# Optimization experiments

Hardware: AMD Instinct MI355X
Metric: run time of the kernel (lower is better)

The kernel has to match this reference:

```python
import jax, jax.numpy as jnp
import numpy as np

NUM_HEADS = 8
OUT_FEATS = 128
D_HEAD = OUT_FEATS // NUM_HEADS
N_NODES = 50000
N_EDGES = 600000
IN_FEATS = 128


def setup_inputs() -> dict:
    key = jax.random.key(0)
    ks = jax.random.split(key, 10)
    h = jax.random.normal(ks[0], (N_NODES, IN_FEATS), dtype=jnp.float32)
    src = jax.random.randint(ks[1], (N_EDGES,), 0, N_NODES)
    dst = jax.random.randint(ks[2], (N_EDGES,), 0, N_NODES)
    s = 1.0 / np.sqrt(IN_FEATS)
    W_Q = jax.random.normal(ks[3], (IN_FEATS, OUT_FEATS), dtype=jnp.float32) * s
    W_K = jax.random.normal(ks[4], (IN_FEATS, OUT_FEATS), dtype=jnp.float32) * s
    W_V = jax.random.normal(ks[5], (IN_FEATS, OUT_FEATS), dtype=jnp.float32) * s
    b_Q = jnp.zeros((OUT_FEATS,), dtype=jnp.float32)
    b_K = jnp.zeros((OUT_FEATS,), dtype=jnp.float32)
    b_V = jnp.zeros((OUT_FEATS,), dtype=jnp.float32)
    return {"h": h, "W_Q": W_Q, "b_Q": b_Q, "W_K": W_K, "b_K": b_K,
            "W_V": W_V, "b_V": b_V, "src": src, "dst": dst}


def _graph_conv(h, W, b, src, dst, norm_src, norm_dst):
    # DGL GraphConv, norm='both': D_dst^{-1/2} * A * D_src^{-1/2} * (h W) + b
    x = (h * norm_src[:, None]) @ W                              # [N, F]
    agg = jax.ops.segment_sum(x[src], dst, num_segments=h.shape[0])
    return agg * norm_dst[:, None] + b


def reference(h, W_Q, b_Q, W_K, b_K, W_V, b_V, src, dst):
    N = h.shape[0]
    ones = jnp.ones(src.shape[0], dtype=h.dtype)
    deg_out = jax.ops.segment_sum(ones, src, num_segments=N)   # out-degree (src side)
    deg_in = jax.ops.segment_sum(ones, dst, num_segments=N)    # in-degree (dst side)
    norm_src = jax.lax.rsqrt(jnp.clip(deg_out, 1.0))
    norm_dst = jax.lax.rsqrt(jnp.clip(deg_in, 1.0))

    Q = jax.nn.relu(_graph_conv(h, W_Q, b_Q, src, dst, norm_src, norm_dst))
    K = jax.nn.relu(_graph_conv(h, W_K, b_K, src, dst, norm_src, norm_dst))
    V = jax.nn.relu(_graph_conv(h, W_V, b_V, src, dst, norm_src, norm_dst))

    Qh = Q.reshape(N, NUM_HEADS, D_HEAD)
    Kh = K.reshape(N, NUM_HEADS, D_HEAD)
    Vh = V.reshape(N, NUM_HEADS, D_HEAD)

    # edge-wise scores: K at src dotted with Q at dst, per head
    score = jnp.sum(Kh[src] * Qh[dst], axis=-1, keepdims=True)   # [E, H, 1]
    score = jnp.exp(jnp.clip(score / np.sqrt(D_HEAD), -10.0, 10.0))

    wV = jax.ops.segment_sum(Vh[src] * score, dst, num_segments=N)  # [N, H, Dh]
    z = jax.ops.segment_sum(score, dst, num_segments=N)             # [N, H, 1]
    return wV / (z + 1e-6)
```

## Files before the change

### kernel.cpp

```cpp
#include <hip/hip_runtime.h>

#define INF  128
#define OUTF 128
#define NH   8
#define DHD  16
#define CAP  48

typedef __attribute__((ext_vector_type(8))) short bf16x8;
typedef __attribute__((ext_vector_type(4))) float f32x4;

__device__ __forceinline__ float bf16_to_f32(unsigned short u) {
    union { unsigned int i; float f; } v;
    v.i = ((unsigned int)u) << 16;
    return v.f;
}
__device__ __forceinline__ unsigned short f32_to_bf16(float f) {
    union { float f; unsigned int i; } v;
    v.f = f;
    unsigned int x = v.i;
    return (unsigned short)((x + 0x7fffu + ((x >> 16) & 1u)) >> 16);
}

__global__ void k_front(const int* __restrict__ src, const int* __restrict__ dst,
                        int* __restrict__ deg_out, int* __restrict__ cursor,
                        int* __restrict__ edge_src, int E, int SB, int HB,
                        const float* __restrict__ h, unsigned short* __restrict__ h_b, int N,
                        const float* __restrict__ Wq, const float* __restrict__ Wk,
                        const float* __restrict__ Wv, unsigned short* __restrict__ frag) {
    if (blockIdx.x < (unsigned)SB) {
        int t = blockIdx.x * 256 + threadIdx.x;
        int e0 = t * 4;
        if (e0 + 4 <= E) {
            int4 s4 = *reinterpret_cast<const int4*>(src + e0);
            int4 d4 = *reinterpret_cast<const int4*>(dst + e0);
            atomicAdd(&deg_out[s4.x], 1);
            atomicAdd(&deg_out[s4.y], 1);
            atomicAdd(&deg_out[s4.z], 1);
            atomicAdd(&deg_out[s4.w], 1);
            int p0 = atomicAdd(&cursor[d4.x], 1);
            int p1 = atomicAdd(&cursor[d4.y], 1);
            int p2 = atomicAdd(&cursor[d4.z], 1);
            int p3 = atomicAdd(&cursor[d4.w], 1);
            if (p0 < CAP) edge_src[d4.x * CAP + p0] = s4.x;
            if (p1 < CAP) edge_src[d4.y * CAP + p1] = s4.y;
            if (p2 < CAP) edge_src[d4.z * CAP + p2] = s4.z;
            if (p3 < CAP) edge_src[d4.w * CAP + p3] = s4.w;
        } else {
            for (int e = e0; e < E; ++e) {
                int s = src[e];
                int d = dst[e];
                atomicAdd(&deg_out[s], 1);
                int p = atomicAdd(&cursor[d], 1);
                if (p < CAP) edge_src[d * CAP + p] = s;
            }
        }
    } else if (blockIdx.x < (unsigned)(SB + HB)) {
        int t = (blockIdx.x - SB) * 256 + threadIdx.x;
        if (t < N * (INF / 8)) {
            const float4* p = reinterpret_cast<const float4*>(h + (size_t)t * 8);
            float4 v0 = p[0], v1 = p[1];
            uint4 o;
            o.x = (unsigned int)f32_to_bf16(v0.x) | ((unsigned int)f32_to_bf16(v0.y) << 16);
            o.y = (unsigned int)f32_to_bf16(v0.z) | ((unsigned int)f32_to_bf16(v0.w) << 16);
            o.z = (unsigned int)f32_to_bf16(v1.x) | ((unsigned int)f32_to_bf16(v1.y) << 16);
            o.w = (unsigned int)f32_to_bf16(v1.z) | ((unsigned int)f32_to_bf16(v1.w) << 16);
            *reinterpret_cast<uint4*>(h_b + (size_t)t * 8) = o;
        }
    } else {
        int t = (blockIdx.x - SB - HB) * 256 + threadIdx.x;
        if (t >= 3 * 8 * 4 * 2 * 64) return;
        int lane  = t & 63;
        int plane = (t >> 6) & 1;
        int ks    = (t >> 7) & 3;
        int nt    = (t >> 9) & 7;
        int mat   = t >> 12;
        const float* W = (mat == 0) ? Wq : ((mat == 1) ? Wk : Wv);
        int ln = lane & 15, quad = lane >> 4;
        int n = nt * 16 + ln;
        unsigned short vals[8];
        #pragma unroll
        for (int j = 0; j < 8; ++j) {
            int k = ks * 32 + quad * 8 + j;
            float a = W[k * OUTF + n];
            unsigned short hb = f32_to_bf16(a);
            vals[j] = plane ? f32_to_bf16(a - bf16_to_f32(hb)) : hb;
        }
        unsigned int* dp = reinterpret_cast<unsigned int*>(frag + (size_t)t * 8);
        #pragma unroll
        for (int j = 0; j < 4; ++j)
            dp[j] = (unsigned int)vals[2 * j] | ((unsigned int)vals[2 * j + 1] << 16);
    }
}

__global__ __launch_bounds__(256) void k_agg(const unsigned short* __restrict__ h_b,
                                             const int* __restrict__ deg_out,
                                             const int* __restrict__ cursor,
                                             const int* __restrict__ edge_src,
                                             float* __restrict__ agg, int N) {
    int wid  = (blockIdx.x * 256 + threadIdx.x) >> 6;
    int lane = threadIdx.x & 63;
    if (wid >= N) return;
    int half = lane >> 5, li = lane & 31;
    int c4 = li * 4;
    float a0 = 0.f, a1 = 0.f, a2 = 0.f, a3 = 0.f;
    int deg = cursor[wid]; if (deg > CAP) deg = CAP;
    const int* row = edge_src + wid * CAP;
    auto proc = [&](int e) {
        int s = row[e];
        int dg = deg_out[s]; if (dg < 1) dg = 1;
        float ns = rsqrtf((float)dg);
        uint2 p = *reinterpret_cast<const uint2*>(h_b + (size_t)s * INF + c4);
        a0 += ns * bf16_to_f32((unsigned short)(p.x & 0xffffu));
        a1 += ns * bf16_to_f32((unsigned short)(p.x >> 16));
        a2 += ns * bf16_to_f32((unsigned short)(p.y & 0xffffu));
        a3 += ns * bf16_to_f32((unsigned short)(p.y >> 16));
    };
    int e = half;
    for (; e + 4 <= deg; e += 4) { proc(e); proc(e + 2); }
    for (; e < deg; e += 2) proc(e);
    a0 += __shfl_xor(a0, 32);
    a1 += __shfl_xor(a1, 32);
    a2 += __shfl_xor(a2, 32);
    a3 += __shfl_xor(a3, 32);
    if (half == 0)
        *reinterpret_cast<float4*>(agg + (size_t)wid * INF + c4) =
            make_float4(a0, a1, a2, a3);
}

__global__ __launch_bounds__(256) void k_gemm(const float* __restrict__ agg,
                                              const unsigned short* __restrict__ frag,
                                              const float* __restrict__ bq,
                                              const float* __restrict__ bk,
                                              const float* __restrict__ bv,
                                              const int* __restrict__ cursor,
                                              float* __restrict__ qbuf,
                                              unsigned short* __restrict__ kvbuf,
                                              int N) {
    int mat = blockIdx.y;
    const float* bb = (mat == 0) ? bq : ((mat == 1) ? bk : bv);

    int wave = threadIdx.x >> 6;
    int lane = threadIdx.x & 63;
    int ln   = lane & 15;
    int quad = lane >> 4;
    int mrow = blockIdx.x * 64 + wave * 16;

    bf16x8 ah[4], al[4];
    {
        int m = mrow + ln; if (m >= N) m = N - 1;
        const float* arow = agg + (size_t)m * INF;
        #pragma unroll
        for (int ks = 0; ks < 4; ++ks) {
            const float4* p = reinterpret_cast<const float4*>(arow + ks * 32 + quad * 8);
            float4 v0 = p[0], v1 = p[1];
            float vv[8] = {v0.x, v0.y, v0.z, v0.w, v1.x, v1.y, v1.z, v1.w};
            #pragma unroll
            for (int j = 0; j < 8; ++j) {
                unsigned short hb = f32_to_bf16(vv[j]);
                ah[ks][j] = (short)hb;
                al[ks][j] = (short)f32_to_bf16(vv[j] - bf16_to_f32(hb));
            }
        }
    }

    float nrm[4];
    #pragma unroll
    for (int r = 0; r < 4; ++r) {
        int m = mrow + quad * 4 + r;
        if (m < N) {
            int dg = cursor[m]; if (dg < 1) dg = 1;
            nrm[r] = rsqrtf((float)dg);
        } else nrm[r] = 0.f;
    }

    #pragma unroll 2
    for (int nt = 0; nt < 8; ++nt) {
        int n0 = nt * 16;
        f32x4 acc = {0.f, 0.f, 0.f, 0.f};
        #pragma unroll
        for (int ks = 0; ks < 4; ++ks) {
            size_t base = ((size_t)(((mat * 8 + nt) * 4 + ks) * 2) * 64 + lane) * 8;
            bf16x8 bh = *reinterpret_cast<const bf16x8*>(frag + base);
            bf16x8 bl = *reinterpret_cast<const bf16x8*>(frag + base + 64 * 8);
            acc = __builtin_amdgcn_mfma_f32_16x16x32_bf16(ah[ks], bh, acc, 0, 0, 0);
            acc = __builtin_amdgcn_mfma_f32_16x16x32_bf16(al[ks], bh, acc, 0, 0, 0);
            acc = __builtin_amdgcn_mfma_f32_16x16x32_bf16(ah[ks], bl, acc, 0, 0, 0);
        }
        int col = n0 + ln;
        float bias = bb[col];
        #pragma unroll
        for (int r = 0; r < 4; ++r) {
            int m = mrow + quad * 4 + r;
            if (m < N) {
                float v = acc[r] * nrm[r] + bias;
                v = (v > 0.f) ? v : 0.f;
                if (mat == 0) {
                    qbuf[(size_t)m * OUTF + col] = v;
                } else {
                    int idx = ((col >> 2) << 3) + (col & 3) + ((mat == 2) ? 4 : 0);
                    kvbuf[(size_t)m * 2 * OUTF + idx] = f32_to_bf16(v);
                }
            }
        }
    }
}

__global__ __launch_bounds__(256) void k_attn(const float* __restrict__ qbuf,
                                              const unsigned short* __restrict__ kvbuf,
                                              const int* __restrict__ cursor,
                                              const int* __restrict__ edge_src,
                                              float* __restrict__ out, int N) {
    int wid  = (blockIdx.x * 256 + threadIdx.x) >> 6;
    int lane = threadIdx.x & 63;
    if (wid >= N) return;
    int half = lane >> 5, li = lane & 31;
    int c4 = li * 4;
    float4 q = *reinterpret_cast<const float4*>(qbuf + (size_t)wid * OUTF + c4);
    float a0 = 0.f, a1 = 0.f, a2 = 0.f, a3 = 0.f, z = 0.f;
    int deg = cursor[wid]; if (deg > CAP) deg = CAP;
    const int* row = edge_src + wid * CAP;
    auto proc = [&](int e) {
        int s = row[e];
        uint4 kp = *reinterpret_cast<const uint4*>(kvbuf + (size_t)s * 2 * OUTF + li * 8);
        float p = q.x * bf16_to_f32((unsigned short)(kp.x & 0xffffu))
                + q.y * bf16_to_f32((unsigned short)(kp.x >> 16))
                + q.z * bf16_to_f32((unsigned short)(kp.y & 0xffffu))
                + q.w * bf16_to_f32((unsigned short)(kp.y >> 16));
        p += __shfl_xor(p, 1);
        p += __shfl_xor(p, 2);
        float w = __expf(fminf(fmaxf(0.25f * p, -10.f), 10.f));
        z  += w;
        a0 += w * bf16_to_f32((unsigned short)(kp.z & 0xffffu));
        a1 += w * bf16_to_f32((unsigned short)(kp.z >> 16));
        a2 += w * bf16_to_f32((unsigned short)(kp.w & 0xffffu));
        a3 += w * bf16_to_f32((unsigned short)(kp.w >> 16));
    };
    int e = half;
    for (; e + 4 <= deg; e += 4) { proc(e); proc(e + 2); }
    for (; e < deg; e += 2) proc(e);
    a0 += __shfl_xor(a0, 32);
    a1 += __shfl_xor(a1, 32);
    a2 += __shfl_xor(a2, 32);
    a3 += __shfl_xor(a3, 32);
    z  += __shfl_xor(z, 32);
    if (half == 0) {
        float inv = 1.0f / (z + 1e-6f);
        *reinterpret_cast<float4*>(out + (size_t)wid * OUTF + c4) =
            make_float4(a0 * inv, a1 * inv, a2 * inv, a3 * inv);
    }
}

extern "C" void kernel_launch(void* const* d_in, const int* in_sizes, int n_in,
                              void* d_out, int out_size, void* d_ws, size_t ws_size,
                              hipStream_t stream) {
    const float* h  = (const float*)d_in[0];
    const float* Wq = (const float*)d_in[1];
    const float* bq = (const float*)d_in[2];
    const float* Wk = (const float*)d_in[3];
    const float* bk = (const float*)d_in[4];
    const float* Wv = (const float*)d_in[5];
    const float* bv = (const float*)d_in[6];
    const int* src = (const int*)d_in[7];
    const int* dst = (const int*)d_in[8];

    const int N = in_sizes[0] / INF;
    const int E = in_sizes[7];

    char* ws = (char*)d_ws;
    size_t off = 0;
    auto carve = [&](size_t bytes) -> void* {
        void* p = ws + off;
        off = (off + bytes + 255) & ~(size_t)255;
        return p;
    };
    int*   zeroed    = (int*)  carve((size_t)2 * N * sizeof(int));
    int*   deg_out   = zeroed;
    int*   cursor    = zeroed + N;
    int*   edge_src  = (int*)  carve((size_t)N * CAP * sizeof(int));
    unsigned short* h_b  = (unsigned short*)carve((size_t)N * INF * sizeof(unsigned short));
    float* agg       = (float*)carve((size_t)N * INF * sizeof(float));
    float* qbuf      = (float*)carve((size_t)N * OUTF * sizeof(float));
    unsigned short* kvbuf = (unsigned short*)carve((size_t)N * 2 * OUTF * sizeof(unsigned short));
    unsigned short* wfrag = (unsigned short*)carve((size_t)3 * 8 * 4 * 2 * 64 * 8 * sizeof(unsigned short));
    (void)ws_size;

    float* out = (float*)d_out;

    hipMemsetAsync(zeroed, 0, (size_t)2 * N * sizeof(int), stream);

    int SB = (E / 4 + 255) / 256 + 1;
    int HB = (N * (INF / 8) + 255) / 256;
    int WB = (3 * 8 * 4 * 2 * 64 + 255) / 256;
    k_front<<<SB + HB + WB, 256, 0, stream>>>(src, dst, deg_out, cursor, edge_src,
                                              E, SB, HB, h, h_b, N, Wq, Wk, Wv, wfrag);

    int gAgg = (N + 3) / 4;
    k_agg<<<gAgg, 256, 0, stream>>>(h_b, deg_out, cursor, edge_src, agg, N);

    dim3 gemm_grid((N + 63) / 64, 3);
    k_gemm<<<gemm_grid, 256, 0, stream>>>(agg, wfrag, bq, bk, bv,
                                          cursor, qbuf, kvbuf, N);

    k_attn<<<gAgg, 256, 0, stream>>>(qbuf, kvbuf, cursor, edge_src, out, N);
}
```

Measured before the change: 272.9 us.

## Fuse neighbor aggregation into GEMM via shared-memory tile, drop agg buffer

Merges the separate aggregation and GEMM kernels into one kernel. Each 64-row block first gathers neighbor features into a padded LDS tile, then runs the MFMA projection for all three weight matrices from that tile. This removes the global fp32 agg round trip (write plus three reads) and one launch. In exchange there are far fewer blocks (N/64 instead of N/4 for the gather), each wave processes 16 rows serially, the gather loop is unrolled further, and 33KB of LDS per block may reduce occupancy and latency hiding for the irregular gather.

```diff
diff --git a/kernel.cpp b/kernel.cpp
--- a/kernel.cpp
+++ b/kernel.cpp
@@ -5,6 +5,7 @@
 #define NH   8
 #define DHD  16
 #define CAP  48
+#define APAD 132
 
 typedef __attribute__((ext_vector_type(8))) short bf16x8;
 typedef __attribute__((ext_vector_type(4))) float f32x4;
@@ -92,113 +93,115 @@
     }
 }
 
-__global__ __launch_bounds__(256) void k_agg(const unsigned short* __restrict__ h_b,
-                                             const int* __restrict__ deg_out,
-                                             const int* __restrict__ cursor,
-                                             const int* __restrict__ edge_src,
-                                             float* __restrict__ agg, int N) {
-    int wid  = (blockIdx.x * 256 + threadIdx.x) >> 6;
-    int lane = threadIdx.x & 63;
-    if (wid >= N) return;
-    int half = lane >> 5, li = lane & 31;
-    int c4 = li * 4;
-    float a0 = 0.f, a1 = 0.f, a2 = 0.f, a3 = 0.f;
-    int deg = cursor[wid]; if (deg > CAP) deg = CAP;
-    const int* row = edge_src + wid * CAP;
-    auto proc = [&](int e) {
-        int s = row[e];
-        int dg = deg_out[s]; if (dg < 1) dg = 1;
-        float ns = rsqrtf((float)dg);
-        uint2 p = *reinterpret_cast<const uint2*>(h_b + (size_t)s * INF + c4);
-        a0 += ns * bf16_to_f32((unsigned short)(p.x & 0xffffu));
-        a1 += ns * bf16_to_f32((unsigned short)(p.x >> 16));
-        a2 += ns * bf16_to_f32((unsigned short)(p.y & 0xffffu));
-        a3 += ns * bf16_to_f32((unsigned short)(p.y >> 16));
-    };
-    int e = half;
-    for (; e + 4 <= deg; e += 4) { proc(e); proc(e + 2); }
-    for (; e < deg; e += 2) proc(e);
-    a0 += __shfl_xor(a0, 32);
-    a1 += __shfl_xor(a1, 32);
-    a2 += __shfl_xor(a2, 32);
-    a3 += __shfl_xor(a3, 32);
-    if (half == 0)
-        *reinterpret_cast<float4*>(agg + (size_t)wid * INF + c4) =
-            make_float4(a0, a1, a2, a3);
-}
-
-__global__ __launch_bounds__(256) void k_gemm(const float* __restrict__ agg,
-                                              const unsigned short* __restrict__ frag,
-                                              const float* __restrict__ bq,
-                                              const float* __restrict__ bk,
-                                              const float* __restrict__ bv,
-                                              const int* __restrict__ cursor,
-                                              float* __restrict__ qbuf,
-                                              unsigned short* __restrict__ kvbuf,
-                                              int N) {
-    int mat = blockIdx.y;
-    const float* bb = (mat == 0) ? bq : ((mat == 1) ? bk : bv);
+__global__ __launch_bounds__(256) void k_aggemm(const unsigned short* __restrict__ h_b,
+                                                const int* __restrict__ deg_out,
+                                                const int* __restrict__ cursor,
+                                                const int* __restrict__ edge_src,
+                                                const unsigned short* __restrict__ frag,
+                                                const float* __restrict__ bq,
+                                                const float* __restrict__ bk,
+                                                const float* __restrict__ bv,
+                                                float* __restrict__ qbuf,
+                                                unsigned short* __restrict__ kvbuf,
+                                                int N) {
+    __shared__ __align__(16) float aggL[64 * APAD];
 
     int wave = threadIdx.x >> 6;
     int lane = threadIdx.x & 63;
+    int mrow = blockIdx.x * 64;
+
+    {
+        int half = lane >> 5, li = lane & 31;
+        int c4 = li * 4;
+        for (int i = 0; i < 16; ++i) {
+            int r = wave * 16 + i;
+            int wid = mrow + r;
+            float a0 = 0.f, a1 = 0.f, a2 = 0.f, a3 = 0.f;
+            if (wid < N) {
+                int deg = cursor[wid]; if (deg > CAP) deg = CAP;
+                const int* row = edge_src + wid * CAP;
+                auto proc = [&](int e) {
+                    int s = row[e];
+                    int dg = deg_out[s]; if (dg < 1) dg = 1;
+                    float ns = rsqrtf((float)dg);
+                    uint2 p = *reinterpret_cast<const uint2*>(h_b + (size_t)s * INF + c4);
+                    a0 += ns * bf16_to_f32((unsigned short)(p.x & 0xffffu));
+                    a1 += ns * bf16_to_f32((unsigned short)(p.x >> 16));
+                    a2 += ns * bf16_to_f32((unsigned short)(p.y & 0xffffu));
+                    a3 += ns * bf16_to_f32((unsigned short)(p.y >> 16));
+                };
+                int e = half;
+                for (; e + 8 <= deg; e += 8) { proc(e); proc(e + 2); proc(e + 4); proc(e + 6); }
+                for (; e < deg; e += 2) proc(e);
+            }
+            a0 += __shfl_xor(a0, 32);
+            a1 += __shfl_xor(a1, 32);
+            a2 += __shfl_xor(a2, 32);
+            a3 += __shfl_xor(a3, 32);
+            if (half == 0)
+                *reinterpret_cast<float4*>(aggL + r * APAD + c4) =
+                    make_float4(a0, a1, a2, a3);
+        }
+    }
+    __syncthreads();
+
     int ln   = lane & 15;
     int quad = lane >> 4;
-    int mrow = blockIdx.x * 64 + wave * 16;
+    int mloc = wave * 16 + ln;
 
     bf16x8 ah[4], al[4];
-    {
-        int m = mrow + ln; if (m >= N) m = N - 1;
-        const float* arow = agg + (size_t)m * INF;
+    #pragma unroll
+    for (int ks = 0; ks < 4; ++ks) {
+        const float4* p = reinterpret_cast<const float4*>(aggL + mloc * APAD + ks * 32 + quad * 8);
+        float4 v0 = p[0], v1 = p[1];
+        float vv[8] = {v0.x, v0.y, v0.z, v0.w, v1.x, v1.y, v1.z, v1.w};
         #pragma unroll
-        for (int ks = 0; ks < 4; ++ks) {
-            const float4* p = reinterpret_cast<const float4*>(arow + ks * 32 + quad * 8);
-            float4 v0 = p[0], v1 = p[1];
-            float vv[8] = {v0.x, v0.y, v0.z, v0.w, v1.x, v1.y, v1.z, v1.w};
-            #pragma unroll
-            for (int j = 0; j < 8; ++j) {
-                unsigned short hb = f32_to_bf16(vv[j]);
-                ah[ks][j] = (short)hb;
-                al[ks][j] = (short)f32_to_bf16(vv[j] - bf16_to_f32(hb));
-            }
+        for (int j = 0; j < 8; ++j) {
+            unsigned short hb = f32_to_bf16(vv[j]);
+            ah[ks][j] = (short)hb;
+            al[ks][j] = (short)f32_to_bf16(vv[j] - bf16_to_f32(hb));
         }
     }
 
     float nrm[4];
     #pragma unroll
     for (int r = 0; r < 4; ++r) {
-        int m = mrow + quad * 4 + r;
+        int m = mrow + wave * 16 + quad * 4 + r;
         if (m < N) {
             int dg = cursor[m]; if (dg < 1) dg = 1;
             nrm[r] = rsqrtf((float)dg);
         } else nrm[r] = 0.f;
     }
 
-    #pragma unroll 2
-    for (int nt = 0; nt < 8; ++nt) {
-        int n0 = nt * 16;
-        f32x4 acc = {0.f, 0.f, 0.f, 0.f};
-        #pragma unroll
-        for (int ks = 0; ks < 4; ++ks) {
-            size_t base = ((size_t)(((mat * 8 + nt) * 4 + ks) * 2) * 64 + lane) * 8;
-            bf16x8 bh = *reinterpret_cast<const bf16x8*>(frag + base);
-            bf16x8 bl = *reinterpret_cast<const bf16x8*>(frag + base + 64 * 8);
-            acc = __builtin_amdgcn_mfma_f32_16x16x32_bf16(ah[ks], bh, acc, 0, 0, 0);
-            acc = __builtin_amdgcn_mfma_f32_16x16x32_bf16(al[ks], bh, acc, 0, 0, 0);
-            acc = __builtin_amdgcn_mfma_f32_16x16x32_bf16(ah[ks], bl, acc, 0, 0, 0);
-        }
-        int col = n0 + ln;
-        float bias = bb[col];
-        #pragma unroll
-        for (int r = 0; r < 4; ++r) {
-            int m = mrow + quad * 4 + r;
-            if (m < N) {
-                float v = acc[r] * nrm[r] + bias;
-                v = (v > 0.f) ? v : 0.f;
-                if (mat == 0) {
-                    qbuf[(size_t)m * OUTF + col] = v;
-                } else {
-                    int idx = ((col >> 2) << 3) + (col & 3) + ((mat == 2) ? 4 : 0);
-                    kvbuf[(size_t)m * 2 * OUTF + idx] = f32_to_bf16(v);
+    for (int mat = 0; mat < 3; ++mat) {
+        const float* bb = (mat == 0) ? bq : ((mat == 1) ? bk : bv);
+        #pragma unroll 2
+        for (int nt = 0; nt < 8; ++nt) {
+            int n0 = nt * 16;
+            f32x4 acc = {0.f, 0.f, 0.f, 0.f};
+            #pragma unroll
+            for (int ks = 0; ks < 4; ++ks) {
+                size_t base = ((size_t)(((mat * 8 + nt) * 4 + ks) * 2) * 64 + lane) * 8;
+                bf16x8 bh = *reinterpret_cast<const bf16x8*>(frag + base);
+                bf16x8 bl = *reinterpret_cast<const bf16x8*>(frag + base + 64 * 8);
+                acc = __builtin_amdgcn_mfma_f32_16x16x32_bf16(ah[ks], bh, acc, 0, 0, 0);
+                acc = __builtin_amdgcn_mfma_f32_16x16x32_bf16(al[ks], bh, acc, 0, 0, 0);
+                acc = __builtin_amdgcn_mfma_f32_16x16x32_bf16(ah[ks], bl, acc, 0, 0, 0);
+            }
+            int col = n0 + ln;
+            float bias = bb[col];
+            #pragma unroll
+            for (int r = 0; r < 4; ++r) {
+                int m = mrow + wave * 16 + quad * 4 + r;
+                if (m < N) {
+                    float v = acc[r] * nrm[r] + bias;
+                    v = (v > 0.f) ? v : 0.f;
+                    if (mat == 0) {
+                        qbuf[(size_t)m * OUTF + col] = v;
+                    } else {
+                        int idx = ((col >> 2) << 3) + (col & 3) + ((mat == 2) ? 4 : 0);
+                        kvbuf[(size_t)m * 2 * OUTF + idx] = f32_to_bf16(v);
+                    }
                 }
             }
         }
@@ -278,7 +281,6 @@
     int*   cursor    = zeroed + N;
     int*   edge_src  = (int*)  carve((size_t)N * CAP * sizeof(int));
     unsigned short* h_b  = (unsigned short*)carve((size_t)N * INF * sizeof(unsigned short));
-    float* agg       = (float*)carve((size_t)N * INF * sizeof(float));
     float* qbuf      = (float*)carve((size_t)N * OUTF * sizeof(float));
     unsigned short* kvbuf = (unsigned short*)carve((size_t)N * 2 * OUTF * sizeof(unsigned short));
     unsigned short* wfrag = (unsigned short*)carve((size_t)3 * 8 * 4 * 2 * 64 * 8 * sizeof(unsigned short));
@@ -294,12 +296,10 @@
     k_front<<<SB + HB + WB, 256, 0, stream>>>(src, dst, deg_out, cursor, edge_src,
                                               E, SB, HB, h, h_b, N, Wq, Wk, Wv, wfrag);
 
+    int gT = (N + 63) / 64;
+    k_aggemm<<<gT, 256, 0, stream>>>(h_b, deg_out, cursor, edge_src, wfrag,
+                                     bq, bk, bv, qbuf, kvbuf, N);
+
     int gAgg = (N + 3) / 4;
-    k_agg<<<gAgg, 256, 0, stream>>>(h_b, deg_out, cursor, edge_src, agg, N);
-
-    dim3 gemm_grid((N + 63) / 64, 3);
-    k_gemm<<<gemm_grid, 256, 0, stream>>>(agg, wfrag, bq, bk, bv,
-                                          cursor, qbuf, kvbuf, N);
-
     k_attn<<<gAgg, 256, 0, stream>>>(qbuf, kvbuf, cursor, edge_src, out, N);
 }
```

New measurement: 286.7 us. 5.0% more time.
